# Kernel optimization log

Measured on AMD Instinct MI355X. Metric: run time of the kernel, lower is better.

## Reference

```python
import jax, jax.numpy as jnp
import numpy as np

B, N, D_IN, D_OUT, H, W = 2, 2048, 1024, 1024, 16, 64
DH = D_OUT // H


def setup_inputs() -> dict:
    key = jax.random.key(0)
    ks = jax.random.split(key, 6)
    x = jax.random.normal(ks[0], (B, N, D_IN), dtype=jnp.float32)
    s_in = 1.0 / np.sqrt(D_IN)
    s_out = 1.0 / np.sqrt(D_OUT)
    wq = jax.random.normal(ks[1], (D_IN, D_OUT), dtype=jnp.float32) * s_in
    wk = jax.random.normal(ks[2], (D_IN, D_OUT), dtype=jnp.float32) * s_in
    wv = jax.random.normal(ks[3], (D_IN, D_OUT), dtype=jnp.float32) * s_in
    wo = jax.random.normal(ks[4], (D_OUT, D_OUT), dtype=jnp.float32) * s_out
    # sparse global tokens: every 256th token is global
    global_attention = (jnp.arange(N)[None, :] % 256 == 0) & jnp.ones((B, 1), bool)
    return {"x": x, "wq": wq, "wk": wk, "wv": wv, "wo": wo,
            "global_attention": global_attention}


def _mask(global_attention):
    # True = masked out. Causal local window + global rows/cols unmasked.
    i = jnp.arange(N)[:, None]
    j = jnp.arange(N)[None, :]
    allowed = (i - j < W) & (i >= j)          # causal sliding window
    local_mask = ~allowed                      # [N, N], True = masked
    g = global_attention                       # [B, N] bool
    # global token j clears row j and column j of the mask
    global_clear = g[:, :, None] | g[:, None, :]   # [B, N, N]
    return local_mask[None, :, :] & ~global_clear  # [B, N, N]


def reference(x, wq, wk, wv, wo, global_attention):
    b, n, _ = x.shape
    q = (x @ wq).reshape(b, n, H, DH).transpose(0, 2, 1, 3)  # [b,h,n,dh]
    k = (x @ wk).reshape(b, n, H, DH).transpose(0, 2, 1, 3)
    v = (x @ wv).reshape(b, n, H, DH).transpose(0, 2, 1, 3)
    scores = jnp.einsum('bhqd,bhkd->bhqk', q, k) / jnp.sqrt(jnp.float32(DH))
    mask = _mask(global_attention)[:, None, :, :]            # [b,1,n,n]
    scores = jnp.where(mask, -jnp.inf, scores)
    attn = jax.nn.softmax(scores, axis=-1)
    ctx = jnp.einsum('bhqk,bhkd->bqhd', attn, v).reshape(b, n, D_OUT)
    return ctx @ wo
```

## Files before the change

### kernel.cpp

```cpp
#include <hip/hip_runtime.h>


using u16 = unsigned short;
using u32 = unsigned int;

typedef __attribute__((ext_vector_type(8))) short bf16x8;
typedef __attribute__((ext_vector_type(4))) float f32x4;

__device__ __forceinline__ float b2f(u16 s) {
  union { u32 u; float f; } x; x.u = ((u32)s) << 16; return x.f;
}
__device__ __forceinline__ u16 f2b(float f) {
  union { float f; u32 u; } x; x.f = f;
  u32 r = (x.u + 0x7fffu + ((x.u >> 16) & 1u)) >> 16;
  return (u16)r;
}

__global__ __launch_bounds__(256) void k_pre(const float* __restrict__ x,
                                             u16* __restrict__ xb,
                                             const float* __restrict__ wq,
                                             const float* __restrict__ wk,
                                             const float* __restrict__ wv,
                                             const float* __restrict__ wo,
                                             u16* __restrict__ wqkvT,
                                             u16* __restrict__ woT) {
  __shared__ float tile[64][65];
  const int bid = blockIdx.x;
  if (bid < 2048) {
    int idx = (bid * 256 + threadIdx.x) * 8;
    float4 a = *(const float4*)(x + idx);
    float4 b = *(const float4*)(x + idx + 4);
    uint4 o;
    o.x = (u32)f2b(a.x) | ((u32)f2b(a.y) << 16);
    o.y = (u32)f2b(a.z) | ((u32)f2b(a.w) << 16);
    o.z = (u32)f2b(b.x) | ((u32)f2b(b.y) << 16);
    o.w = (u32)f2b(b.z) | ((u32)f2b(b.w) << 16);
    *(uint4*)(xb + idx) = o;
  } else {
    const int id = bid - 2048;
    const int z = id >> 8, xy = id & 255;
    const float* src = (z == 0) ? wq : (z == 1) ? wk : (z == 2) ? wv : wo;
    u16* dst = (z < 3) ? (wqkvT + ((size_t)z << 20)) : woT;
    const int n0 = (xy & 15) * 64, k0 = (xy >> 4) * 64;
    const int tx = threadIdx.x & 63, ty = threadIdx.x >> 6;
    #pragma unroll
    for (int r = 0; r < 64; r += 4)
      tile[r + ty][tx] = src[(size_t)(k0 + r + ty) * 1024 + n0 + tx];
    __syncthreads();
    #pragma unroll
    for (int r = 0; r < 64; r += 4)
      dst[(size_t)(n0 + r + ty) * 1024 + k0 + tx] = f2b(tile[tx][r + ty]);
  }
}

__device__ __forceinline__ void gload16(const u16* g, u16* l) {
  __builtin_amdgcn_global_load_lds((const __attribute__((address_space(1))) void*)g,
                                   (__attribute__((address_space(3))) void*)l, 16, 0, 0);
}

template<int F32OUT>
__global__ __launch_bounds__(256, 3) void k_gemm128(const u16* __restrict__ A,
                                                    const u16* __restrict__ Bt,
                                                    void* __restrict__ C, int N, int K) {
  __shared__ u16 lds[3][2][4096];
  const int t = threadIdx.x;
  const int wid = t >> 6, lane = t & 63;
  const int l4 = lane >> 4, l16 = lane & 15;
  const int wr = wid >> 1, wc = wid & 1;
  const int d = blockIdx.y * gridDim.x + blockIdx.x;
  const int qq = (gridDim.x * gridDim.y) >> 3;
  const int tau = (d & 7) * qq + (d >> 3);
  const int bn = tau % gridDim.x, bm = tau / gridDim.x;
  const u16* Ab = A + (size_t)bm * 128 * K;
  const u16* Bb = Bt + (size_t)bn * 128 * K;
  const int srow0 = t >> 2;
  const int scol = (((t & 3) ^ ((t >> 3) & 3)) << 3);
  const int sdst = wid << 9;
  const int sl8 = ((l4 ^ ((l16 >> 1) & 3)) << 3);
  const int NT = K >> 5;
  f32x4 acc[4][4] = {};

  #pragma unroll
  for (int pt = 0; pt < 2; ++pt) {
    #pragma unroll
    for (int c = 0; c < 2; ++c) {
      int r = c * 64 + srow0;
      gload16(Ab + (size_t)r * K + (pt << 5) + scol, &lds[pt][0][c * 2048 + sdst]);
      gload16(Bb + (size_t)r * K + (pt << 5) + scol, &lds[pt][1][c * 2048 + sdst]);
    }
  }

  int cur = 0, nxt2 = 2;
  for (int tt = 0; tt < NT; ++tt) {
    if (tt + 1 < NT) asm volatile("s_waitcnt vmcnt(4)" ::: "memory");
    else             asm volatile("s_waitcnt vmcnt(0)" ::: "memory");
    __builtin_amdgcn_s_barrier();
    if (tt + 2 < NT) {
      const int k0 = (tt + 2) << 5;
      u16* dA = &lds[nxt2][0][sdst];
      u16* dB = &lds[nxt2][1][sdst];
      #pragma unroll
      for (int c = 0; c < 2; ++c) {
        int r = c * 64 + srow0;
        gload16(Ab + (size_t)r * K + k0 + scol, dA + c * 2048);
        gload16(Bb + (size_t)r * K + k0 + scol, dB + c * 2048);
      }
    }
    const u16* As = lds[cur][0];
    const u16* Bs = lds[cur][1];
    bf16x8 af[4], bf[4];
    #pragma unroll
    for (int m = 0; m < 4; ++m)
      af[m] = *(const bf16x8*)&As[(wr * 64 + m * 16 + l16) * 32 + sl8];
    #pragma unroll
    for (int n = 0; n < 4; ++n)
      bf[n] = *(const bf16x8*)&Bs[(wc * 64 + n * 16 + l16) * 32 + sl8];
    __builtin_amdgcn_s_setprio(1);
    #pragma unroll
    for (int m = 0; m < 4; ++m)
      #pragma unroll
      for (int n = 0; n < 4; ++n)
        acc[m][n] = __builtin_amdgcn_mfma_f32_16x16x32_bf16(af[m], bf[n], acc[m][n], 0, 0, 0);
    __builtin_amdgcn_s_setprio(0);
    cur = (cur == 2) ? 0 : cur + 1;
    nxt2 = (nxt2 == 2) ? 0 : nxt2 + 1;
  }

  #pragma unroll
  for (int m = 0; m < 4; ++m) {
    const int row0 = bm * 128 + wr * 64 + m * 16 + l4 * 4;
    #pragma unroll
    for (int n = 0; n < 4; ++n) {
      const int col = bn * 128 + wc * 64 + n * 16 + l16;
      #pragma unroll
      for (int r = 0; r < 4; ++r) {
        if (F32OUT) ((float*)C)[(size_t)(row0 + r) * N + col] = acc[m][n][r];
        else        ((u16*)C)[(size_t)(row0 + r) * N + col] = f2b(acc[m][n][r]);
      }
    }
  }
}

template<int F32OUT, int GRED>
__global__ __launch_bounds__(256, 2) void k_gemm64(const u16* __restrict__ A,
                                                   const u16* __restrict__ Bt,
                                                   void* __restrict__ C, int N, int K,
                                                   const float* __restrict__ gpart,
                                                   u16* __restrict__ ctxw) {
  __shared__ u16 lds[3][6144];
  const int t = threadIdx.x;
  const int wid = t >> 6, lane = t & 63;
  const int l4 = lane >> 4, l16 = lane & 15;
  const int wr = wid >> 1, wc = wid & 1;
  const int d = blockIdx.y * gridDim.x + blockIdx.x;
  const int qq = (gridDim.x * gridDim.y) >> 3;
  const int tau = (d & 7) * qq + (d >> 3);
  const int bn = tau % gridDim.x, bm = tau / gridDim.x;
  const u16* Ab = A + (size_t)bm * 64 * K;
  const u16* Bb = Bt + (size_t)bn * 128 * K;
  const int srow0 = t >> 2;
  const int scol = (((t & 3) ^ ((t >> 3) & 3)) << 3);
  const int sdst = wid << 9;
  const int sl8 = ((l4 ^ ((l16 >> 1) & 3)) << 3);
  const int NT = K >> 5;
  f32x4 acc[2][4] = {};

  if (GRED && (bm & 3) == 0) {
    const int bb = bm >> 5;
    const int irow = (bm & 31) * 64;
    const int row8 = (bm & 31) >> 2;
    const int h = t >> 4;
    const int d0 = (t & 15) * 4;
    const float* g0 = gpart + ((size_t)(bb * 16 + h) * 32) * 520;
    float o0 = 0.f, o1 = 0.f, o2 = 0.f, o3 = 0.f, ls = 0.f;
    for (int q = 0; q < 32; ++q) {
      const float4 v = *(const float4*)(g0 + q * 520 + row8 * 64 + d0);
      o0 += v.x; o1 += v.y; o2 += v.z; o3 += v.w;
      ls += g0[q * 520 + 512 + row8];
    }
    const float inv = 1.f / ls;
    u16* cw = ctxw + ((size_t)(bb * 2048 + irow)) * 1024 + h * 64 + d0;
    cw[0] = f2b(o0 * inv); cw[1] = f2b(o1 * inv);
    cw[2] = f2b(o2 * inv); cw[3] = f2b(o3 * inv);
    __syncthreads();
  }

  #pragma unroll
  for (int pt = 0; pt < 2; ++pt) {
    gload16(Ab + (size_t)srow0 * K + (pt << 5) + scol, &lds[pt][sdst]);
    #pragma unroll
    for (int c = 0; c < 2; ++c)
      gload16(Bb + (size_t)(c * 64 + srow0) * K + (pt << 5) + scol,
              &lds[pt][2048 + c * 2048 + sdst]);
  }

  int cur = 0, nxt2 = 2;
  for (int tt = 0; tt < NT; ++tt) {
    if (tt + 1 < NT) asm volatile("s_waitcnt vmcnt(3)" ::: "memory");
    else             asm volatile("s_waitcnt vmcnt(0)" ::: "memory");
    __builtin_amdgcn_s_barrier();
    if (tt + 2 < NT) {
      const int k0 = (tt + 2) << 5;
      u16* dst = &lds[nxt2][0];
      gload16(Ab + (size_t)srow0 * K + k0 + scol, dst + sdst);
      #pragma unroll
      for (int c = 0; c < 2; ++c)
        gload16(Bb + (size_t)(c * 64 + srow0) * K + k0 + scol, dst + 2048 + c * 2048 + sdst);
    }
    const u16* As = lds[cur];
    const u16* Bs = lds[cur] + 2048;
    bf16x8 af[2], bf[4];
    #pragma unroll
    for (int m = 0; m < 2; ++m)
      af[m] = *(const bf16x8*)&As[(wr * 32 + m * 16 + l16) * 32 + sl8];
    #pragma unroll
    for (int n = 0; n < 4; ++n)
      bf[n] = *(const bf16x8*)&Bs[(wc * 64 + n * 16 + l16) * 32 + sl8];
    __builtin_amdgcn_s_setprio(1);
    #pragma unroll
    for (int m = 0; m < 2; ++m)
      #pragma unroll
      for (int n = 0; n < 4; ++n)
        acc[m][n] = __builtin_amdgcn_mfma_f32_16x16x32_bf16(af[m], bf[n], acc[m][n], 0, 0, 0);
    __builtin_amdgcn_s_setprio(0);
    cur = (cur == 2) ? 0 : cur + 1;
    nxt2 = (nxt2 == 2) ? 0 : nxt2 + 1;
  }

  #pragma unroll
  for (int m = 0; m < 2; ++m) {
    const int row0 = bm * 64 + wr * 32 + m * 16 + l4 * 4;
    #pragma unroll
    for (int n = 0; n < 4; ++n) {
      const int col = bn * 128 + wc * 64 + n * 16 + l16;
      #pragma unroll
      for (int r = 0; r < 4; ++r) {
        if (F32OUT) ((float*)C)[(size_t)(row0 + r) * N + col] = acc[m][n][r];
        else        ((u16*)C)[(size_t)(row0 + r) * N + col] = f2b(acc[m][n][r]);
      }
    }
  }
}

__global__ __launch_bounds__(256) void k_attn_tile(const u16* __restrict__ qkv,
                                                   u16* __restrict__ ctx,
                                                   float* __restrict__ gpart) {
  __shared__ u16 buf[26880];
  __shared__ u16 Qgs[16 * 72];
  __shared__ u16 Pgs[16 * 72];
  __shared__ float lred[4][16];
  u16* Qs = buf;
  u16* Ks = buf + 4608;
  u16* Vt = buf + 16128;
  u16* Ps = buf;

  const int t = threadIdx.x, wid = t >> 6, lane = t & 63;
  const int l4 = lane >> 4, l16 = lane & 15;
  const int qt = blockIdx.x, h = blockIdx.y, b = blockIdx.z;
  const int q0 = qt * 64;
  const int kbase = q0 - 64;
  const size_t base = (size_t)b * 2048 * 3072;
  const u16* Qg = qkv + base + h * 64;
  const u16* Kg = qkv + base + 1024 + h * 64;
  const u16* Vg = qkv + base + 2048 + h * 64;

  for (int s = t; s < 512; s += 256) {
    int r = s >> 3, c = (s & 7) * 8;
    *(uint4*)&Qs[r * 72 + c] = *(const uint4*)&Qg[(size_t)(q0 + r) * 3072 + c];
  }
  if (t < 128) {
    int r = t >> 3, c = (t & 7) * 8;
    if (r < 8) {
      *(uint4*)&Qgs[r * 72 + c] = *(const uint4*)&Qg[(size_t)(r * 256) * 3072 + c];
    } else {
      uint4 z = {0, 0, 0, 0};
      *(uint4*)&Qgs[r * 72 + c] = z;
    }
  }
  for (int s = t; s < 1088; s += 256) {
    int r = s >> 3, c = (s & 7) * 8;
    int j = (r < 128) ? max(kbase + r, 0) : (r - 128) * 256;
    *(uint4*)&Ks[r * 72 + c] = *(const uint4*)&Kg[(size_t)j * 3072 + c];
  }
  for (int s = t; s < 1088; s += 256) {
    int r = s >> 3, c = (s & 7) * 8;
    int j = (r < 128) ? max(kbase + r, 0) : (r - 128) * 256;
    uint4 v = *(const uint4*)&Vg[(size_t)j * 3072 + c];
    const u16* pv = (const u16*)&v;
    const int ch = r >> 3;
    #pragma unroll
    for (int e8 = 0; e8 < 8; ++e8) {
      const int d = c + e8;
      const int kd = ((d >> 3) ^ d) & 7;
      const int chs = (ch < 16) ? (ch ^ kd) : ch;
      Vt[d * 168 + chs * 8 + (r & 7)] = pv[e8];
    }
  }
  for (int z = t; z < 64 * 24; z += 256) {
    int d = z / 24, j = 136 + z % 24;
    Vt[d * 168 + j] = 0;
  }
  __syncthreads();

  f32x4 sa[10] = {};
  #pragma unroll
  for (int ks = 0; ks < 2; ++ks) {
    bf16x8 qa = *(const bf16x8*)&Qs[(wid * 16 + l16) * 72 + ks * 32 + l4 * 8];
    #pragma unroll
    for (int n = 0; n < 10; ++n) {
      bf16x8 kb = *(const bf16x8*)&Ks[(n * 16 + l16) * 72 + ks * 32 + l4 * 8];
      sa[n] = __builtin_amdgcn_mfma_f32_16x16x32_bf16(qa, kb, sa[n], 0, 0, 0);
    }
  }

  f32x4 sg = {};
  #pragma unroll
  for (int ks = 0; ks < 2; ++ks) {
    bf16x8 qa = *(const bf16x8*)&Qgs[l16 * 72 + ks * 32 + l4 * 8];
    bf16x8 kb = *(const bf16x8*)&Ks[(64 + wid * 16 + l16) * 72 + ks * 32 + l4 * 8];
    sg = __builtin_amdgcn_mfma_f32_16x16x32_bf16(qa, kb, sg, 0, 0, 0);
  }
  #pragma unroll
  for (int r = 0; r < 4; ++r) {
    float p = __expf(sg[r] * 0.125f);
    sg[r] = p;
    #pragma unroll
    for (int o = 1; o < 16; o <<= 1) p += __shfl_xor(p, o);
    if (l16 == 0) lred[wid][l4 * 4 + r] = p;
  }
  #pragma unroll
  for (int r = 0; r < 4; ++r)
    Pgs[(l4 * 4 + r) * 72 + wid * 16 + l16] = f2b(sg[r]);

  const int qi0 = wid * 16 + l4 * 4;
  #pragma unroll
  for (int n = 0; n < 10; ++n) {
    const int jc = n * 16 + l16;
    #pragma unroll
    for (int r = 0; r < 4; ++r) {
      const int qi = qi0 + r;
      bool allowed;
      if (n < 8) {
        const int kr = kbase + jc;
        allowed = (jc > qi) && (jc <= qi + 64) && (kr >= 0) && ((kr & 255) != 0);
      } else {
        allowed = (jc < 136);
      }
      sa[n][r] = allowed ? sa[n][r] * 0.125f : -1e30f;
    }
  }

  float m[4], l[4];
  #pragma unroll
  for (int r = 0; r < 4; ++r) {
    float mx = sa[0][r];
    #pragma unroll
    for (int n = 1; n < 10; ++n) mx = fmaxf(mx, sa[n][r]);
    #pragma unroll
    for (int o = 1; o < 16; o <<= 1) mx = fmaxf(mx, __shfl_xor(mx, o));
    m[r] = mx;
    l[r] = 0.f;
  }
  #pragma unroll
  for (int n = 0; n < 10; ++n)
    #pragma unroll
    for (int r = 0; r < 4; ++r) {
      float p = __expf(sa[n][r] - m[r]);
      sa[n][r] = p;
      l[r] += p;
    }
  #pragma unroll
  for (int r = 0; r < 4; ++r)
    #pragma unroll
    for (int o = 1; o < 16; o <<= 1) l[r] += __shfl_xor(l[r], o);

  __syncthreads();

  u16* Pw = Ps + wid * (16 * 168);
  #pragma unroll
  for (int n = 0; n < 10; ++n)
    #pragma unroll
    for (int r = 0; r < 4; ++r)
      Pw[(l4 * 4 + r) * 168 + n * 16 + l16] = f2b(sa[n][r]);
  __syncthreads();

  f32x4 o[4] = {};
  #pragma unroll
  for (int ks = 0; ks < 5; ++ks) {
    bf16x8 pa = *(const bf16x8*)&Pw[l16 * 168 + ks * 32 + l4 * 8];
    #pragma unroll
    for (int dt = 0; dt < 4; ++dt) {
      const int dvo = dt * 16 + l16;
      const int kdo = ((dvo >> 3) ^ dvo) & 7;
      const int ch = ks * 4 + l4;
      const int chs = (ch < 16) ? (ch ^ kdo) : ch;
      bf16x8 vb = *(const bf16x8*)&Vt[dvo * 168 + chs * 8];
      o[dt] = __builtin_amdgcn_mfma_f32_16x16x32_bf16(pa, vb, o[dt], 0, 0, 0);
    }
  }

  f32x4 og = {};
  {
    const int dV = wid * 16 + l16;
    const int kdg = ((dV >> 3) ^ dV) & 7;
    #pragma unroll
    for (int ks = 0; ks < 2; ++ks) {
      bf16x8 pa = *(const bf16x8*)&Pgs[l16 * 72 + ks * 32 + l4 * 8];
      const int chs = (8 + ks * 4 + l4) ^ kdg;
      bf16x8 vb = *(const bf16x8*)&Vt[dV * 168 + chs * 8];
      og = __builtin_amdgcn_mfma_f32_16x16x32_bf16(pa, vb, og, 0, 0, 0);
    }
  }
  float* gp = gpart + ((size_t)(b * 16 + h) * 32 + qt) * 520;
  #pragma unroll
  for (int r = 0; r < 4; ++r) {
    int row = l4 * 4 + r;
    if (row < 8) gp[row * 64 + wid * 16 + l16] = og[r];
  }
  if (t < 8) gp[512 + t] = lred[0][t] + lred[1][t] + lred[2][t] + lred[3][t];

  #pragma unroll
  for (int r = 0; r < 4; ++r) {
    const int q = q0 + qi0 + r;
    if ((q & 255) == 0) continue;
    const float inv = 1.0f / l[r];
    #pragma unroll
    for (int dt = 0; dt < 4; ++dt)
      ctx[(size_t)(b * 2048 + q) * 1024 + h * 64 + dt * 16 + l16] = f2b(o[dt][r] * inv);
  }
}

extern "C" void kernel_launch(void* const* d_in, const int* in_sizes, int n_in,
                              void* d_out, int out_size, void* d_ws, size_t ws_size,
                              hipStream_t stream) {
  (void)in_sizes; (void)n_in; (void)out_size; (void)ws_size;
  const float* x  = (const float*)d_in[0];
  const float* wq = (const float*)d_in[1];
  const float* wk = (const float*)d_in[2];
  const float* wv = (const float*)d_in[3];
  const float* wo = (const float*)d_in[4];
  char* ws = (char*)d_ws;
  u16* xb    = (u16*)(ws);
  u16* qkv   = (u16*)(ws + (8u  << 20));
  u16* ctx   = (u16*)(ws + (32u << 20));
  u16* wqkvT = (u16*)(ws + (40u << 20));
  u16* woT   = (u16*)(ws + (46u << 20));
  float* gpart = (float*)(ws);

  k_pre<<<3072, 256, 0, stream>>>(x, xb, wq, wk, wv, wo, wqkvT, woT);
  k_gemm128<0><<<dim3(24, 32), 256, 0, stream>>>(xb, wqkvT, qkv, 3072, 1024);
  k_attn_tile<<<dim3(32, 16, 2), 256, 0, stream>>>(qkv, ctx, gpart);
  k_gemm64<1, 1><<<dim3(8, 64), 256, 0, stream>>>(ctx, woT, d_out, 1024, 1024, gpart, ctx);
}
```

Measured before the change: 88.09 us.

## Fuse fp32-to-bf16 conversion of x into the QKV GEMM A-tile loads

Result: no change. 89.01 us (+1.0%).

```diff
diff --git a/kernel.cpp b/kernel.cpp
--- a/kernel.cpp
+++ b/kernel.cpp
@@ -15,42 +15,30 @@
   u32 r = (x.u + 0x7fffu + ((x.u >> 16) & 1u)) >> 16;
   return (u16)r;
 }
-
-__global__ __launch_bounds__(256) void k_pre(const float* __restrict__ x,
-                                             u16* __restrict__ xb,
-                                             const float* __restrict__ wq,
+__device__ __forceinline__ u32 cvtpk(float lo, float hi) {
+  u32 r; asm("v_cvt_pk_bf16_f32 %0, %1, %2" : "=v"(r) : "v"(lo), "v"(hi)); return r;
+}
+
+__global__ __launch_bounds__(256) void k_pre(const float* __restrict__ wq,
                                              const float* __restrict__ wk,
                                              const float* __restrict__ wv,
                                              const float* __restrict__ wo,
                                              u16* __restrict__ wqkvT,
                                              u16* __restrict__ woT) {
   __shared__ float tile[64][65];
-  const int bid = blockIdx.x;
-  if (bid < 2048) {
-    int idx = (bid * 256 + threadIdx.x) * 8;
-    float4 a = *(const float4*)(x + idx);
-    float4 b = *(const float4*)(x + idx + 4);
-    uint4 o;
-    o.x = (u32)f2b(a.x) | ((u32)f2b(a.y) << 16);
-    o.y = (u32)f2b(a.z) | ((u32)f2b(a.w) << 16);
-    o.z = (u32)f2b(b.x) | ((u32)f2b(b.y) << 16);
-    o.w = (u32)f2b(b.z) | ((u32)f2b(b.w) << 16);
-    *(uint4*)(xb + idx) = o;
-  } else {
-    const int id = bid - 2048;
-    const int z = id >> 8, xy = id & 255;
-    const float* src = (z == 0) ? wq : (z == 1) ? wk : (z == 2) ? wv : wo;
-    u16* dst = (z < 3) ? (wqkvT + ((size_t)z << 20)) : woT;
-    const int n0 = (xy & 15) * 64, k0 = (xy >> 4) * 64;
-    const int tx = threadIdx.x & 63, ty = threadIdx.x >> 6;
-    #pragma unroll
-    for (int r = 0; r < 64; r += 4)
-      tile[r + ty][tx] = src[(size_t)(k0 + r + ty) * 1024 + n0 + tx];
-    __syncthreads();
-    #pragma unroll
-    for (int r = 0; r < 64; r += 4)
-      dst[(size_t)(n0 + r + ty) * 1024 + k0 + tx] = f2b(tile[tx][r + ty]);
-  }
+  const int id = blockIdx.x;
+  const int z = id >> 8, xy = id & 255;
+  const float* src = (z == 0) ? wq : (z == 1) ? wk : (z == 2) ? wv : wo;
+  u16* dst = (z < 3) ? (wqkvT + ((size_t)z << 20)) : woT;
+  const int n0 = (xy & 15) * 64, k0 = (xy >> 4) * 64;
+  const int tx = threadIdx.x & 63, ty = threadIdx.x >> 6;
+  #pragma unroll
+  for (int r = 0; r < 64; r += 4)
+    tile[r + ty][tx] = src[(size_t)(k0 + r + ty) * 1024 + n0 + tx];
+  __syncthreads();
+  #pragma unroll
+  for (int r = 0; r < 64; r += 4)
+    dst[(size_t)(n0 + r + ty) * 1024 + k0 + tx] = f2b(tile[tx][r + ty]);
 }
 
 __device__ __forceinline__ void gload16(const u16* g, u16* l) {
@@ -58,11 +46,11 @@
                                    (__attribute__((address_space(3))) void*)l, 16, 0, 0);
 }
 
-template<int F32OUT>
-__global__ __launch_bounds__(256, 3) void k_gemm128(const u16* __restrict__ A,
-                                                    const u16* __restrict__ Bt,
-                                                    void* __restrict__ C, int N, int K) {
+__global__ __launch_bounds__(256, 3) void k_qkv(const float* __restrict__ X,
+                                                const u16* __restrict__ Bt,
+                                                u16* __restrict__ C) {
   __shared__ u16 lds[3][2][4096];
+  const int K = 1024, N = 3072, NT = 32;
   const int t = threadIdx.x;
   const int wid = t >> 6, lane = t & 63;
   const int l4 = lane >> 4, l16 = lane & 15;
@@ -71,60 +59,89 @@
   const int qq = (gridDim.x * gridDim.y) >> 3;
   const int tau = (d & 7) * qq + (d >> 3);
   const int bn = tau % gridDim.x, bm = tau / gridDim.x;
-  const u16* Ab = A + (size_t)bm * 128 * K;
+  const float* Ax = X + (size_t)bm * 128 * K;
   const u16* Bb = Bt + (size_t)bn * 128 * K;
   const int srow0 = t >> 2;
   const int scol = (((t & 3) ^ ((t >> 3) & 3)) << 3);
   const int sdst = wid << 9;
+  const int adst = (wid << 9) + (lane << 3);
   const int sl8 = ((l4 ^ ((l16 >> 1) & 3)) << 3);
-  const int NT = K >> 5;
   f32x4 acc[4][4] = {};
-
-  #pragma unroll
-  for (int pt = 0; pt < 2; ++pt) {
-    #pragma unroll
-    for (int c = 0; c < 2; ++c) {
-      int r = c * 64 + srow0;
-      gload16(Ab + (size_t)r * K + (pt << 5) + scol, &lds[pt][0][c * 2048 + sdst]);
-      gload16(Bb + (size_t)r * K + (pt << 5) + scol, &lds[pt][1][c * 2048 + sdst]);
-    }
-  }
-
-  int cur = 0, nxt2 = 2;
-  for (int tt = 0; tt < NT; ++tt) {
-    if (tt + 1 < NT) asm volatile("s_waitcnt vmcnt(4)" ::: "memory");
+  float4 fa0[2][2], fa1[2][2];
+
+  int c0 = 0, c1 = 1, c2 = 2;
+
+  #define QKV_ISSUE(FA, BUF, KT)                                                  \
+    { const int k0_ = (KT) << 5;                                                  \
+      _Pragma("unroll")                                                           \
+      for (int c = 0; c < 2; ++c) {                                               \
+        const float* ap = Ax + (size_t)(c * 64 + srow0) * K + k0_ + scol;         \
+        FA[c][0] = *(const float4*)ap;                                            \
+        FA[c][1] = *(const float4*)(ap + 4);                                      \
+        gload16(Bb + (size_t)(c * 64 + srow0) * K + k0_ + scol,                   \
+                &lds[BUF][1][c * 2048 + sdst]);                                   \
+      } }
+
+  #define QKV_WRITE(FA, BUF)                                                      \
+    { _Pragma("unroll")                                                           \
+      for (int c = 0; c < 2; ++c) {                                               \
+        union { u32 w[4]; uint4 v; } u_;                                          \
+        u_.w[0] = cvtpk(FA[c][0].x, FA[c][0].y);                                  \
+        u_.w[1] = cvtpk(FA[c][0].z, FA[c][0].w);                                  \
+        u_.w[2] = cvtpk(FA[c][1].x, FA[c][1].y);                                  \
+        u_.w[3] = cvtpk(FA[c][1].z, FA[c][1].w);                                  \
+        *(uint4*)&lds[BUF][0][c * 2048 + adst] = u_.v;                            \
+      } }
+
+  #define QKV_COMPUTE(BUF)                                                        \
+    { const u16* As = lds[BUF][0];                                                \
+      const u16* Bs = lds[BUF][1];                                                \
+      bf16x8 af[4], bf[4];                                                        \
+      _Pragma("unroll")                                                           \
+      for (int m = 0; m < 4; ++m)                                                 \
+        af[m] = *(const bf16x8*)&As[(wr * 64 + m * 16 + l16) * 32 + sl8];         \
+      _Pragma("unroll")                                                           \
+      for (int n = 0; n < 4; ++n)                                                 \
+        bf[n] = *(const bf16x8*)&Bs[(wc * 64 + n * 16 + l16) * 32 + sl8];         \
+      __builtin_amdgcn_s_setprio(1);                                              \
+      _Pragma("unroll")                                                           \
+      for (int m = 0; m < 4; ++m)                                                 \
+        _Pragma("unroll")                                                         \
+        for (int n = 0; n < 4; ++n)                                               \
+          acc[m][n] = __builtin_amdgcn_mfma_f32_16x16x32_bf16(af[m], bf[n],       \
+                                                              acc[m][n], 0, 0, 0);\
+      __builtin_amdgcn_s_setprio(0); }
+
+  QKV_ISSUE(fa0, 0, 0);
+  QKV_ISSUE(fa1, 1, 1);
+  QKV_WRITE(fa0, 0);
+  asm volatile("s_waitcnt vmcnt(6)" ::: "memory");
+  asm volatile("s_waitcnt lgkmcnt(0)" ::: "memory");
+  __builtin_amdgcn_s_barrier();
+
+  for (int tt = 0; tt < NT; tt += 2) {
+    QKV_WRITE(fa1, c1);
+    if (tt + 2 < NT) QKV_ISSUE(fa0, c2, tt + 2);
+    QKV_COMPUTE(c0);
+    if (tt + 2 < NT) asm volatile("s_waitcnt vmcnt(6)" ::: "memory");
     else             asm volatile("s_waitcnt vmcnt(0)" ::: "memory");
+    asm volatile("s_waitcnt lgkmcnt(0)" ::: "memory");
     __builtin_amdgcn_s_barrier();
+    { int tmp = c0; c0 = c1; c1 = c2; c2 = tmp; }
+    if (tt + 2 < NT) QKV_WRITE(fa0, c1);
+    if (tt + 3 < NT) QKV_ISSUE(fa1, c2, tt + 3);
+    QKV_COMPUTE(c0);
     if (tt + 2 < NT) {
-      const int k0 = (tt + 2) << 5;
-      u16* dA = &lds[nxt2][0][sdst];
-      u16* dB = &lds[nxt2][1][sdst];
-      #pragma unroll
-      for (int c = 0; c < 2; ++c) {
-        int r = c * 64 + srow0;
-        gload16(Ab + (size_t)r * K + k0 + scol, dA + c * 2048);
-        gload16(Bb + (size_t)r * K + k0 + scol, dB + c * 2048);
-      }
-    }
-    const u16* As = lds[cur][0];
-    const u16* Bs = lds[cur][1];
-    bf16x8 af[4], bf[4];
-    #pragma unroll
-    for (int m = 0; m < 4; ++m)
-      af[m] = *(const bf16x8*)&As[(wr * 64 + m * 16 + l16) * 32 + sl8];
-    #pragma unroll
-    for (int n = 0; n < 4; ++n)
-      bf[n] = *(const bf16x8*)&Bs[(wc * 64 + n * 16 + l16) * 32 + sl8];
-    __builtin_amdgcn_s_setprio(1);
-    #pragma unroll
-    for (int m = 0; m < 4; ++m)
-      #pragma unroll
-      for (int n = 0; n < 4; ++n)
-        acc[m][n] = __builtin_amdgcn_mfma_f32_16x16x32_bf16(af[m], bf[n], acc[m][n], 0, 0, 0);
-    __builtin_amdgcn_s_setprio(0);
-    cur = (cur == 2) ? 0 : cur + 1;
-    nxt2 = (nxt2 == 2) ? 0 : nxt2 + 1;
-  }
+      if (tt + 3 < NT) asm volatile("s_waitcnt vmcnt(6)" ::: "memory");
+      else             asm volatile("s_waitcnt vmcnt(0)" ::: "memory");
+      asm volatile("s_waitcnt lgkmcnt(0)" ::: "memory");
+      __builtin_amdgcn_s_barrier();
+      { int tmp = c0; c0 = c1; c1 = c2; c2 = tmp; }
+    }
+  }
+  #undef QKV_ISSUE
+  #undef QKV_WRITE
+  #undef QKV_COMPUTE
 
   #pragma unroll
   for (int m = 0; m < 4; ++m) {
@@ -133,10 +150,8 @@
     for (int n = 0; n < 4; ++n) {
       const int col = bn * 128 + wc * 64 + n * 16 + l16;
       #pragma unroll
-      for (int r = 0; r < 4; ++r) {
-        if (F32OUT) ((float*)C)[(size_t)(row0 + r) * N + col] = acc[m][n][r];
-        else        ((u16*)C)[(size_t)(row0 + r) * N + col] = f2b(acc[m][n][r]);
-      }
+      for (int r = 0; r < 4; ++r)
+        C[(size_t)(row0 + r) * N + col] = f2b(acc[m][n][r]);
     }
   }
 }
@@ -440,15 +455,14 @@
   const float* wv = (const float*)d_in[3];
   const float* wo = (const float*)d_in[4];
   char* ws = (char*)d_ws;
-  u16* xb    = (u16*)(ws);
   u16* qkv   = (u16*)(ws + (8u  << 20));
   u16* ctx   = (u16*)(ws + (32u << 20));
   u16* wqkvT = (u16*)(ws + (40u << 20));
   u16* woT   = (u16*)(ws + (46u << 20));
   float* gpart = (float*)(ws);
 
-  k_pre<<<3072, 256, 0, stream>>>(x, xb, wq, wk, wv, wo, wqkvT, woT);
-  k_gemm128<0><<<dim3(24, 32), 256, 0, stream>>>(xb, wqkvT, qkv, 3072, 1024);
+  k_pre<<<1024, 256, 0, stream>>>(wq, wk, wv, wo, wqkvT, woT);
+  k_qkv<<<dim3(24, 32), 256, 0, stream>>>(x, wqkvT, qkv);
   k_attn_tile<<<dim3(32, 16, 2), 256, 0, stream>>>(qkv, ctx, gpart);
   k_gemm64<1, 1><<<dim3(8, 64), 256, 0, stream>>>(ctx, woT, d_out, 1024, 1024, gpart, ctx);
 }
```

## Replace QKV projection GEMM with 256x256-tile, 8-wave ping-pong pipelined kernel

Applied to the files above, without the earlier changes.

New measurement: 86.63 us. No clear change (-1.7%).

```diff
diff --git a/kernel.cpp b/kernel.cpp
--- a/kernel.cpp
+++ b/kernel.cpp
@@ -58,87 +58,119 @@
                                    (__attribute__((address_space(3))) void*)l, 16, 0, 0);
 }
 
-template<int F32OUT>
-__global__ __launch_bounds__(256, 3) void k_gemm128(const u16* __restrict__ A,
-                                                    const u16* __restrict__ Bt,
-                                                    void* __restrict__ C, int N, int K) {
-  __shared__ u16 lds[3][2][4096];
+__global__ __launch_bounds__(512, 2) void k_qkv256(const u16* __restrict__ A,
+                                                   const u16* __restrict__ Bt,
+                                                   u16* __restrict__ C) {
+  __shared__ __attribute__((aligned(16))) u16 lds[65536];
+  const int K = 1024, N = 3072, NT = 16;
   const int t = threadIdx.x;
   const int wid = t >> 6, lane = t & 63;
   const int l4 = lane >> 4, l16 = lane & 15;
-  const int wr = wid >> 1, wc = wid & 1;
+  const int qr = wid >> 2, qc = wid & 3;
   const int d = blockIdx.y * gridDim.x + blockIdx.x;
   const int qq = (gridDim.x * gridDim.y) >> 3;
   const int tau = (d & 7) * qq + (d >> 3);
   const int bn = tau % gridDim.x, bm = tau / gridDim.x;
-  const u16* Ab = A + (size_t)bm * 128 * K;
-  const u16* Bb = Bt + (size_t)bn * 128 * K;
-  const int srow0 = t >> 2;
-  const int scol = (((t & 3) ^ ((t >> 3) & 3)) << 3);
-  const int sdst = wid << 9;
-  const int sl8 = ((l4 ^ ((l16 >> 1) & 3)) << 3);
-  const int NT = K >> 5;
-  f32x4 acc[4][4] = {};
-
-  #pragma unroll
-  for (int pt = 0; pt < 2; ++pt) {
-    #pragma unroll
-    for (int c = 0; c < 2; ++c) {
-      int r = c * 64 + srow0;
-      gload16(Ab + (size_t)r * K + (pt << 5) + scol, &lds[pt][0][c * 2048 + sdst]);
-      gload16(Bb + (size_t)r * K + (pt << 5) + scol, &lds[pt][1][c * 2048 + sdst]);
-    }
-  }
-
-  int cur = 0, nxt2 = 2;
+  const u16* Ab = A + (size_t)bm * 256 * K;
+  const u16* Bb = Bt + (size_t)bn * 256 * K;
+  const int rowbase = wid * 8 + (lane >> 3);
+  const int scc = ((lane & 7) ^ ((lane >> 3) & 7)) << 3;
+  const int sdst = wid << 6;
+  const int rsw = (l16 & 7);
+  f32x4 acc[2][2][4][2] = {};
+  bf16x8 af[4][2], bf0[2][2], bf1[2][2];
+
+  #define STG(G, BUF, KT, H)                                                       \
+    { const u16* gb = (G) ? Bb : Ab;                                               \
+      u16* lb = lds + ((G) ? 32768 : 0) + (BUF) * 16384 + ((H) * 1024 + sdst) * 8; \
+      _Pragma("unroll")                                                            \
+      for (int i = 0; i < 2; ++i)                                                  \
+        gload16(gb + (size_t)((H) * 128 + i * 64 + rowbase) * K + (KT) * 64 + scc, \
+                lb + i * 4096); }
+
+  #define LOAD_A(AS, MH)                                                           \
+    { _Pragma("unroll")                                                            \
+      for (int m = 0; m < 4; ++m) {                                                \
+        const int ro = (MH) * 128 + qr * 64 + m * 16 + l16;                        \
+        _Pragma("unroll")                                                          \
+        for (int ks = 0; ks < 2; ++ks)                                             \
+          af[m][ks] = *(const bf16x8*)&(AS)[ro * 64 + (((ks * 4 + l4) ^ rsw) << 3)]; \
+      } }
+
+  #define LOAD_B(BS, BF, NH)                                                       \
+    { _Pragma("unroll")                                                            \
+      for (int n = 0; n < 2; ++n) {                                                \
+        const int ro = (NH) * 128 + qc * 32 + n * 16 + l16;                        \
+        _Pragma("unroll")                                                          \
+        for (int ks = 0; ks < 2; ++ks)                                             \
+          BF[n][ks] = *(const bf16x8*)&(BS)[ro * 64 + (((ks * 4 + l4) ^ rsw) << 3)]; \
+      } }
+
+  #define QUAD(MH, NH, BF)                                                         \
+    { __builtin_amdgcn_s_setprio(1);                                               \
+      _Pragma("unroll")                                                            \
+      for (int m = 0; m < 4; ++m)                                                  \
+        _Pragma("unroll")                                                          \
+        for (int n = 0; n < 2; ++n) {                                              \
+          f32x4 c = acc[MH][NH][m][n];                                             \
+          c = __builtin_amdgcn_mfma_f32_16x16x32_bf16(af[m][0], BF[n][0], c, 0, 0, 0); \
+          c = __builtin_amdgcn_mfma_f32_16x16x32_bf16(af[m][1], BF[n][1], c, 0, 0, 0); \
+          acc[MH][NH][m][n] = c;                                                   \
+        }                                                                          \
+      __builtin_amdgcn_s_setprio(0); }
+
+  STG(0, 0, 0, 0); STG(1, 0, 0, 0); STG(0, 0, 0, 1); STG(1, 0, 0, 1);
+  STG(0, 1, 1, 0); STG(1, 1, 1, 0);
+  asm volatile("s_waitcnt vmcnt(4)" ::: "memory");
+  __builtin_amdgcn_s_barrier();
+
   for (int tt = 0; tt < NT; ++tt) {
-    if (tt + 1 < NT) asm volatile("s_waitcnt vmcnt(4)" ::: "memory");
-    else             asm volatile("s_waitcnt vmcnt(0)" ::: "memory");
-    __builtin_amdgcn_s_barrier();
-    if (tt + 2 < NT) {
-      const int k0 = (tt + 2) << 5;
-      u16* dA = &lds[nxt2][0][sdst];
-      u16* dB = &lds[nxt2][1][sdst];
+    const int beta = tt & 1;
+    const u16* As = lds + beta * 16384;
+    const u16* Bs = lds + 32768 + beta * 16384;
+    LOAD_A(As, 0);
+    LOAD_B(Bs, bf0, 0);
+    if (tt + 1 < NT) STG(0, beta ^ 1, tt + 1, 1);
+    __builtin_amdgcn_s_barrier();
+    QUAD(0, 0, bf0);
+    __builtin_amdgcn_s_barrier();
+    LOAD_B(Bs, bf1, 1);
+    if (tt + 1 < NT) STG(1, beta ^ 1, tt + 1, 1);
+    __builtin_amdgcn_s_barrier();
+    QUAD(0, 1, bf1);
+    __builtin_amdgcn_s_barrier();
+    LOAD_A(As, 1);
+    if (tt + 2 < NT) STG(0, beta, tt + 2, 0);
+    __builtin_amdgcn_s_barrier();
+    QUAD(1, 0, bf0);
+    __builtin_amdgcn_s_barrier();
+    if (tt + 2 < NT) STG(1, beta, tt + 2, 0);
+    __builtin_amdgcn_s_barrier();
+    QUAD(1, 1, bf1);
+    if (tt + 2 < NT)      asm volatile("s_waitcnt vmcnt(4)" ::: "memory");
+    else if (tt + 1 < NT) asm volatile("s_waitcnt vmcnt(0)" ::: "memory");
+    __builtin_amdgcn_s_barrier();
+  }
+  #undef STG
+  #undef LOAD_A
+  #undef LOAD_B
+  #undef QUAD
+
+  #pragma unroll
+  for (int mh = 0; mh < 2; ++mh)
+    #pragma unroll
+    for (int m = 0; m < 4; ++m) {
+      const int row0 = bm * 256 + mh * 128 + qr * 64 + m * 16 + l4 * 4;
       #pragma unroll
-      for (int c = 0; c < 2; ++c) {
-        int r = c * 64 + srow0;
-        gload16(Ab + (size_t)r * K + k0 + scol, dA + c * 2048);
-        gload16(Bb + (size_t)r * K + k0 + scol, dB + c * 2048);
-      }
-    }
-    const u16* As = lds[cur][0];
-    const u16* Bs = lds[cur][1];
-    bf16x8 af[4], bf[4];
-    #pragma unroll
-    for (int m = 0; m < 4; ++m)
-      af[m] = *(const bf16x8*)&As[(wr * 64 + m * 16 + l16) * 32 + sl8];
-    #pragma unroll
-    for (int n = 0; n < 4; ++n)
-      bf[n] = *(const bf16x8*)&Bs[(wc * 64 + n * 16 + l16) * 32 + sl8];
-    __builtin_amdgcn_s_setprio(1);
-    #pragma unroll
-    for (int m = 0; m < 4; ++m)
-      #pragma unroll
-      for (int n = 0; n < 4; ++n)
-        acc[m][n] = __builtin_amdgcn_mfma_f32_16x16x32_bf16(af[m], bf[n], acc[m][n], 0, 0, 0);
-    __builtin_amdgcn_s_setprio(0);
-    cur = (cur == 2) ? 0 : cur + 1;
-    nxt2 = (nxt2 == 2) ? 0 : nxt2 + 1;
-  }
-
-  #pragma unroll
-  for (int m = 0; m < 4; ++m) {
-    const int row0 = bm * 128 + wr * 64 + m * 16 + l4 * 4;
-    #pragma unroll
-    for (int n = 0; n < 4; ++n) {
-      const int col = bn * 128 + wc * 64 + n * 16 + l16;
-      #pragma unroll
-      for (int r = 0; r < 4; ++r) {
-        if (F32OUT) ((float*)C)[(size_t)(row0 + r) * N + col] = acc[m][n][r];
-        else        ((u16*)C)[(size_t)(row0 + r) * N + col] = f2b(acc[m][n][r]);
-      }
-    }
-  }
+      for (int nh = 0; nh < 2; ++nh)
+        #pragma unroll
+        for (int n = 0; n < 2; ++n) {
+          const int col = bn * 256 + nh * 128 + qc * 32 + n * 16 + l16;
+          #pragma unroll
+          for (int r = 0; r < 4; ++r)
+            C[(size_t)(row0 + r) * N + col] = f2b(acc[mh][nh][m][n][r]);
+        }
+    }
 }
 
 template<int F32OUT, int GRED>
@@ -448,7 +480,7 @@
   float* gpart = (float*)(ws);
 
   k_pre<<<3072, 256, 0, stream>>>(x, xb, wq, wk, wv, wo, wqkvT, woT);
-  k_gemm128<0><<<dim3(24, 32), 256, 0, stream>>>(xb, wqkvT, qkv, 3072, 1024);
+  k_qkv256<<<dim3(12, 16), 512, 0, stream>>>(xb, wqkvT, qkv);
   k_attn_tile<<<dim3(32, 16, 2), 256, 0, stream>>>(qkv, ctx, gpart);
   k_gemm64<1, 1><<<dim3(8, 64), 256, 0, stream>>>(ctx, woT, d_out, 1024, 1024, gpart, ctx);
 }
```
